# Performance work log

Hardware: AMD Instinct MI355X
Metric: run time of the kernel (lower is better)

The kernel has to match this reference:

```python
import jax, jax.numpy as jnp
import numpy as np

CLIP_DIM = 1024
X_DIM = 768
NUM_HEADS = 8
HEAD_DIM = X_DIM // NUM_HEADS
SCALE = HEAD_DIM ** -0.5
EPS1 = 1e-6  # custom channel-first LayerNorm
EPS2 = 1e-5  # nn.LayerNorm default


def setup_inputs() -> dict:
    key = jax.random.key(0)
    ks = jax.random.split(key, 12)
    B, H, W = 8, 32, 32
    d = X_DIM
    inp = {
        "x": jax.random.normal(ks[0], (B, H, W, d), jnp.float32),
        "clip_features": jax.random.normal(ks[1], (B, CLIP_DIM, 16, 16), jnp.float32),
        "conv_w": jax.random.normal(ks[2], (CLIP_DIM, d), jnp.float32) * (CLIP_DIM ** -0.5),
        "conv_b": jnp.zeros((d,), jnp.float32),
        "ln1_w": jnp.ones((d,), jnp.float32),
        "ln1_b": jnp.zeros((d,), jnp.float32),
        "wq": jax.random.normal(ks[3], (d, d), jnp.float32) * (d ** -0.5),
        "bq": jnp.zeros((d,), jnp.float32),
        "wk": jax.random.normal(ks[4], (d, d), jnp.float32) * (d ** -0.5),
        "bk": jnp.zeros((d,), jnp.float32),
        "wv": jax.random.normal(ks[5], (d, d), jnp.float32) * (d ** -0.5),
        "bv": jnp.zeros((d,), jnp.float32),
        "wo": jax.random.normal(ks[6], (d, d), jnp.float32) * (d ** -0.5),
        "bo": jnp.zeros((d,), jnp.float32),
        "ln2_w": jnp.ones((d,), jnp.float32),
        "ln2_b": jnp.zeros((d,), jnp.float32),
    }
    return inp


def _forward(x, clip_features, conv_w, conv_b, ln1_w, ln1_b,
             wq, bq, wk, bk, wv, bv, wo, bo, ln2_w, ln2_b):
    B, H, W, d = x.shape
    S = H * W
    # bilinear resize (align_corners=False == half-pixel, jax default)
    clip_r = jax.image.resize(clip_features, (B, CLIP_DIM, H, W), method="bilinear")
    # 1x1 conv: bchw,cd->bdhw
    c = jnp.einsum("bchw,cd->bdhw", clip_r, conv_w) + conv_b[None, :, None, None]
    # channel-first LayerNorm over dim 1
    u = c.mean(1, keepdims=True)
    s = ((c - u) ** 2).mean(1, keepdims=True)
    c = (c - u) * jax.lax.rsqrt(s + EPS1)
    c = ln1_w[None, :, None, None] * c + ln1_b[None, :, None, None]
    # to (B, S, d)
    q_in = jnp.transpose(c, (0, 2, 3, 1)).reshape(B, S, d)
    kv_in = x.reshape(B, S, d)
    # projections -> (B, h, S, hd)
    def heads(t):
        return jnp.transpose(t.reshape(B, S, NUM_HEADS, HEAD_DIM), (0, 2, 1, 3))
    q = heads(q_in @ wq + bq)
    k = heads(kv_in @ wk + bk)
    v = heads(kv_in @ wv + bv)
    scores = jnp.einsum("bhqd,bhkd->bhqk", q, k) * SCALE
    attn = jax.nn.softmax(scores, axis=-1)
    o = jnp.einsum("bhqk,bhkd->bhqd", attn, v)
    o = jnp.transpose(o, (0, 2, 1, 3)).reshape(B, S, d)
    o = o @ wo + bo
    # standard LayerNorm over last dim
    mu = o.mean(-1, keepdims=True)
    var = ((o - mu) ** 2).mean(-1, keepdims=True)
    o = (o - mu) * jax.lax.rsqrt(var + EPS2) * ln2_w + ln2_b
    return o.reshape(B, H, W, d)


def reference(x, clip_features, conv_w, conv_b, ln1_w, ln1_b,
              wq, bq, wk, bk, wv, bv, wo, bo, ln2_w, ln2_b):
    return _forward(x, clip_features, conv_w, conv_b, ln1_w, ln1_b,
                    wq, bq, wk, bk, wv, bv, wo, bo, ln2_w, ln2_b)
```

## Files before the change

kernel.cpp:

```cpp
#include <hip/hip_runtime.h>
#include <hip/hip_bf16.h>

typedef __attribute__((ext_vector_type(8))) short short8;
typedef __attribute__((ext_vector_type(4))) short short4v;
typedef __attribute__((ext_vector_type(4))) float floatx4;
typedef unsigned short u16;

__device__ __forceinline__ float b2f(u16 u) {
    unsigned int x = ((unsigned int)u) << 16;
    float f;
    __builtin_memcpy(&f, &x, 4);
    return f;
}
__device__ __forceinline__ u16 f2b(float f) {
    unsigned int x;
    __builtin_memcpy(&x, &f, 4);
    unsigned int lsb = (x >> 16) & 1u;
    x += 0x7fffu + lsb;
    return (u16)(x >> 16);
}

__device__ __forceinline__ void gload16(const u16* g, u16* l) {
    __builtin_amdgcn_global_load_lds(
        (const __attribute__((address_space(1))) void*)g,
        (__attribute__((address_space(3))) void*)l,
        16, 0, 0);
}

__global__ __launch_bounds__(256) void transpose_f2b(const float* __restrict__ in,
                                                     u16* __restrict__ out,
                                                     int R, int C, long ibs, long obs) {
    __shared__ float tile[32][33];
    int b = blockIdx.z;
    const float* ip = in + (long)b * ibs;
    u16* op = out + (long)b * obs;
    int c0 = blockIdx.x * 32, r0 = blockIdx.y * 32;
    int tx = threadIdx.x & 31, ty = threadIdx.x >> 5;
    for (int j = 0; j < 32; j += 8)
        tile[ty + j][tx] = ip[(long)(r0 + ty + j) * C + c0 + tx];
    __syncthreads();
    for (int j = 0; j < 32; j += 8)
        op[(long)(c0 + ty + j) * R + r0 + tx] = f2b(tile[tx][ty + j]);
}

__global__ __launch_bounds__(256) void transpose_w4(const float* __restrict__ w0,
                                                    const float* __restrict__ w1,
                                                    const float* __restrict__ w2,
                                                    const float* __restrict__ w3,
                                                    u16* __restrict__ outbase) {
    __shared__ float tile[32][33];
    int z = blockIdx.z;
    const float* ip = (z == 0) ? w0 : (z == 1) ? w1 : (z == 2) ? w2 : w3;
    u16* op = outbase + (long)z * 589824;
    int c0 = blockIdx.x * 32, r0 = blockIdx.y * 32;
    int tx = threadIdx.x & 31, ty = threadIdx.x >> 5;
    for (int j = 0; j < 32; j += 8)
        tile[ty + j][tx] = ip[(long)(r0 + ty + j) * 768 + c0 + tx];
    __syncthreads();
    for (int j = 0; j < 32; j += 8)
        op[(long)(c0 + ty + j) * 768 + r0 + tx] = f2b(tile[tx][ty + j]);
}

__global__ __launch_bounds__(256) void cast_f2b(const float* __restrict__ in,
                                                u16* __restrict__ out, int n8) {
    int i = blockIdx.x * 256 + threadIdx.x;
    if (i < n8) {
        float4 f0 = ((const float4*)in)[i * 2];
        float4 f1 = ((const float4*)in)[i * 2 + 1];
        short8 s;
        s[0] = (short)f2b(f0.x); s[1] = (short)f2b(f0.y);
        s[2] = (short)f2b(f0.z); s[3] = (short)f2b(f0.w);
        s[4] = (short)f2b(f1.x); s[5] = (short)f2b(f1.y);
        s[6] = (short)f2b(f1.z); s[7] = (short)f2b(f1.w);
        ((short8*)out)[i] = s;
    }
}

__global__ __launch_bounds__(256) void gemm_ld64(const u16* __restrict__ A,
                                                 const u16* __restrict__ Bt,
                                                 const float* __restrict__ bias,
                                                 u16* __restrict__ Cv,
                                                 int M, int N, int K, int ldc,
                                                 float oscale) {
    __shared__ __align__(16) u16 lA[128 * 64];
    __shared__ __align__(16) u16 lB[64 * 64];
    int tid = threadIdx.x, lane = tid & 63, w = tid >> 6;
    int m0 = blockIdx.x * 128, n0 = blockIdx.y * 64;
    floatx4 acc[2][4] = {};
    const int lr = lane & 15, kg = lane >> 4;
    int rt = tid >> 3, sl = ((tid & 7) ^ (rt & 7)) * 8;
    const u16* gA0 = &A[(long)(m0 + rt) * K + sl];
    const u16* gA1 = &A[(long)(m0 + 32 + rt) * K + sl];
    const u16* gA2 = &A[(long)(m0 + 64 + rt) * K + sl];
    const u16* gA3 = &A[(long)(m0 + 96 + rt) * K + sl];
    const u16* gB0 = &Bt[(long)(n0 + rt) * K + sl];
    const u16* gB1 = &Bt[(long)(n0 + 32 + rt) * K + sl];
    const int s0 = (kg ^ (lr & 7)) * 8;
    for (int k0 = 0; k0 < K; k0 += 64) {
        gload16(gA0 + k0, &lA[w * 512]);
        gload16(gA1 + k0, &lA[2048 + w * 512]);
        gload16(gA2 + k0, &lA[4096 + w * 512]);
        gload16(gA3 + k0, &lA[6144 + w * 512]);
        gload16(gB0 + k0, &lB[w * 512]);
        gload16(gB1 + k0, &lB[2048 + w * 512]);
        __syncthreads();
        #pragma unroll
        for (int ks = 0; ks < 2; ks++) {
            int sseg = s0 ^ (ks << 5);
            short8 a0 = *(const short8*)&lA[(w * 32 + lr) * 64 + sseg];
            short8 a1 = *(const short8*)&lA[(w * 32 + 16 + lr) * 64 + sseg];
            #pragma unroll
            for (int ni = 0; ni < 4; ni++) {
                short8 bf = *(const short8*)&lB[(ni * 16 + lr) * 64 + sseg];
                acc[0][ni] = __builtin_amdgcn_mfma_f32_16x16x32_bf16(a0, bf, acc[0][ni], 0, 0, 0);
                acc[1][ni] = __builtin_amdgcn_mfma_f32_16x16x32_bf16(a1, bf, acc[1][ni], 0, 0, 0);
            }
        }
        __syncthreads();
    }
    #pragma unroll
    for (int mi = 0; mi < 2; mi++)
        #pragma unroll
        for (int ni = 0; ni < 4; ni++) {
            int n = n0 + ni * 16 + lr;
            float bv = bias[n];
            #pragma unroll
            for (int r = 0; r < 4; r++) {
                int m = m0 + w * 32 + mi * 16 + kg * 4 + r;
                Cv[(long)m * ldc + n] = f2b((acc[mi][ni][r] + bv) * oscale);
            }
        }
}

__global__ __launch_bounds__(256) void gemm128kv(const u16* __restrict__ A,
                                                 const u16* __restrict__ Bt,
                                                 const float* __restrict__ biasA,
                                                 const float* __restrict__ biasB,
                                                 u16* __restrict__ Cv,
                                                 u16* __restrict__ vTout,
                                                 int M, int N, int K, int ldc) {
    __shared__ __align__(16) u16 lA[128 * 64];
    __shared__ __align__(16) u16 lB[128 * 64];
    int tid = threadIdx.x, lane = tid & 63, w = tid >> 6;
    int wr = w >> 1, wc = w & 1;
    int m0 = blockIdx.x * 128, n0 = blockIdx.y * 128;
    floatx4 acc[4][4] = {};
    const int lr = lane & 15, kg = lane >> 4;
    int rt = tid >> 3, sl = ((tid & 7) ^ (rt & 7)) * 8;
    const u16* gA0 = &A[(long)(m0 + rt) * K + sl];
    const u16* gA1 = &A[(long)(m0 + 32 + rt) * K + sl];
    const u16* gA2 = &A[(long)(m0 + 64 + rt) * K + sl];
    const u16* gA3 = &A[(long)(m0 + 96 + rt) * K + sl];
    const u16* gB0 = &Bt[(long)(n0 + rt) * K + sl];
    const u16* gB1 = &Bt[(long)(n0 + 32 + rt) * K + sl];
    const u16* gB2 = &Bt[(long)(n0 + 64 + rt) * K + sl];
    const u16* gB3 = &Bt[(long)(n0 + 96 + rt) * K + sl];
    const int s0 = (kg ^ (lr & 7)) * 8;
    for (int k0 = 0; k0 < K; k0 += 64) {
        gload16(gA0 + k0, &lA[w * 512]);
        gload16(gA1 + k0, &lA[2048 + w * 512]);
        gload16(gA2 + k0, &lA[4096 + w * 512]);
        gload16(gA3 + k0, &lA[6144 + w * 512]);
        gload16(gB0 + k0, &lB[w * 512]);
        gload16(gB1 + k0, &lB[2048 + w * 512]);
        gload16(gB2 + k0, &lB[4096 + w * 512]);
        gload16(gB3 + k0, &lB[6144 + w * 512]);
        __syncthreads();
        #pragma unroll
        for (int ks = 0; ks < 2; ks++) {
            int sseg = s0 ^ (ks << 5);
            short8 af[4], bf[4];
            #pragma unroll
            for (int mi = 0; mi < 4; mi++)
                af[mi] = *(const short8*)&lA[(wr * 64 + mi * 16 + lr) * 64 + sseg];
            #pragma unroll
            for (int ni = 0; ni < 4; ni++)
                bf[ni] = *(const short8*)&lB[(wc * 64 + ni * 16 + lr) * 64 + sseg];
            #pragma unroll
            for (int mi = 0; mi < 4; mi++)
                #pragma unroll
                for (int ni = 0; ni < 4; ni++)
                    acc[mi][ni] = __builtin_amdgcn_mfma_f32_16x16x32_bf16(af[mi], bf[ni], acc[mi][ni], 0, 0, 0);
        }
        __syncthreads();
    }
    #pragma unroll
    for (int mi = 0; mi < 4; mi++)
        #pragma unroll
        for (int ni = 0; ni < 4; ni++) {
            int n = n0 + wc * 64 + ni * 16 + lr;
            float bv = (n < 768) ? biasA[n] : biasB[n - 768];
            if (n >= 768) {
                int fg = n - 768;
                int h = fg / 96, f = fg - h * 96;
                int mb = m0 + wr * 64 + mi * 16 + kg * 4;
                long vrow = ((long)((m0 >> 10) * 8 + h) * 96 + f) * 1024 + (mb & 1023);
                short4v pk;
                #pragma unroll
                for (int r = 0; r < 4; r++) pk[r] = (short)f2b(acc[mi][ni][r] + bv);
                *(short4v*)&vTout[vrow] = pk;
            } else {
                #pragma unroll
                for (int r = 0; r < 4; r++) {
                    int m = m0 + wr * 64 + mi * 16 + kg * 4 + r;
                    Cv[(long)m * ldc + n] = f2b(acc[mi][ni][r] + bv);
                }
            }
        }
}

__global__ __launch_bounds__(256) void ln1_resize_w(const u16* __restrict__ t_lo,
                                                    const float* __restrict__ lnw,
                                                    const float* __restrict__ lnb,
                                                    u16* __restrict__ q_in) {
    int wv = threadIdx.x >> 6, lane = threadIdx.x & 63;
    int b = blockIdx.z, oh = blockIdx.y, ow = blockIdx.x * 4 + wv;
    float sy = oh * 0.5f - 0.25f;
    int iy = (int)floorf(sy);
    float fy = sy - (float)iy;
    int y0 = min(max(iy, 0), 15), y1 = min(max(iy + 1, 0), 15);
    float sx = ow * 0.5f - 0.25f;
    int ix = (int)floorf(sx);
    float fx = sx - (float)ix;
    int x0 = min(max(ix, 0), 15), x1 = min(max(ix + 1, 0), 15);
    float w00 = (1.f - fy) * (1.f - fx), w01 = (1.f - fy) * fx;
    float w10 = fy * (1.f - fx), w11 = fy * fx;
    long base = (long)b * 256 * 768;
    long i00 = base + (long)(y0 * 16 + x0) * 768;
    long i01 = base + (long)(y0 * 16 + x1) * 768;
    long i10 = base + (long)(y1 * 16 + x0) * 768;
    long i11 = base + (long)(y1 * 16 + x1) * 768;
    float v[12];
    float s = 0.f, sq = 0.f;
    #pragma unroll
    for (int j = 0; j < 3; j++) {
        int c0 = (j * 64 + lane) * 4;
        short4v a = *(const short4v*)&t_lo[i00 + c0];
        short4v c = *(const short4v*)&t_lo[i01 + c0];
        short4v d = *(const short4v*)&t_lo[i10 + c0];
        short4v e = *(const short4v*)&t_lo[i11 + c0];
        #pragma unroll
        for (int k = 0; k < 4; k++) {
            float val = w00 * b2f((u16)a[k]) + w01 * b2f((u16)c[k]) +
                        w10 * b2f((u16)d[k]) + w11 * b2f((u16)e[k]);
            v[j * 4 + k] = val;
            s += val;
            sq += val * val;
        }
    }
    #pragma unroll
    for (int off = 32; off >= 1; off >>= 1) {
        s += __shfl_xor(s, off);
        sq += __shfl_xor(sq, off);
    }
    float mean = s * (1.f / 768.f);
    float var = sq * (1.f / 768.f) - mean * mean;
    float rstd = rsqrtf(var + 1e-6f);
    long orow = ((long)b * 1024 + oh * 32 + ow) * 768;
    #pragma unroll
    for (int j = 0; j < 3; j++) {
        int c0 = (j * 64 + lane) * 4;
        float4 w4 = *(const float4*)&lnw[c0];
        float4 b4 = *(const float4*)&lnb[c0];
        short4v o;
        o[0] = (short)f2b((v[j * 4 + 0] - mean) * rstd * w4.x + b4.x);
        o[1] = (short)f2b((v[j * 4 + 1] - mean) * rstd * w4.y + b4.y);
        o[2] = (short)f2b((v[j * 4 + 2] - mean) * rstd * w4.z + b4.z);
        o[3] = (short)f2b((v[j * 4 + 3] - mean) * rstd * w4.w + b4.w);
        *(short4v*)&q_in[orow + c0] = o;
    }
}

#define PP 76
__global__ __launch_bounds__(512) void attn_kernel(const u16* __restrict__ Q,
                                                   const u16* __restrict__ Km,
                                                   const u16* __restrict__ Vt,
                                                   u16* __restrict__ O) {
    __shared__ __align__(16) u16 lK[2 * 4096];
    __shared__ __align__(16) u16 lKb[2 * 2048];
    __shared__ __align__(16) u16 lV[2 * 6144];
    __shared__ __align__(16) u16 lP[128 * PP];
    int tid = threadIdx.x, lane = tid & 63, w = tid >> 6;
    int L = blockIdx.x + (blockIdx.y << 3) + (blockIdx.z << 6);
    int b = L & 7, h = (L >> 3) & 7, qt = L >> 6;
    const int lr = lane & 15, kg = lane >> 4;

    long qrow = ((long)b * 1024 + qt * 128 + w * 16 + lr) * 768 + h * 96;
    short8 aq[3];
    for (int ks = 0; ks < 3; ks++) aq[ks] = *(const short8*)&Q[qrow + ks * 32 + kg * 8];

    floatx4 acco[6] = {};
    float lrun[4] = {0.f, 0.f, 0.f, 0.f};

    long kvbase = ((long)b * 1024) * 768 + h * 96;
    long vtbase = ((long)(b * 8 + h)) * 96 * 1024;

    const u16* gp[3];
    u16* lp[3];
    int gs[3], bs[3];
    #pragma unroll
    for (int i = 0; i < 3; i++) {
        int id = tid + i * 512;
        if (id < 512) {
            int row = id >> 3, lg = (id & 7) ^ (row & 7);
            lp[i] = &lK[id * 8];
            gp[i] = &Km[kvbase + (long)row * 768 + lg * 8];
            gs[i] = 64 * 768;
            bs[i] = 4096;
        } else if (id < 768) {
            int j = id - 512;
            int row = j >> 2, lg = (j & 3) ^ (row & 3);
            lp[i] = &lKb[j * 8];
            gp[i] = &Km[kvbase + (long)row * 768 + 64 + lg * 8];
            gs[i] = 64 * 768;
            bs[i] = 2048;
        } else {
            int j = id - 768;
            int f = j >> 3, lg = (j & 7) ^ (f & 7);
            lp[i] = &lV[j * 8];
            gp[i] = &Vt[vtbase + (long)f * 1024 + lg * 8];
            gs[i] = 64;
            bs[i] = 6144;
        }
    }

    const int sA = (kg ^ (lr & 7)) * 8;
    const int sB = (kg ^ (lr & 3)) * 8;

    #pragma unroll
    for (int i = 0; i < 3; i++) {
        gload16(gp[i], lp[i]);
        gp[i] += gs[i];
    }

    for (int kt = 0; kt < 16; kt++) {
        int cur = kt & 1, nxt = cur ^ 1;
        if (kt < 15) {
            #pragma unroll
            for (int i = 0; i < 3; i++) {
                gload16(gp[i], lp[i] + nxt * bs[i]);
                gp[i] += gs[i];
            }
            asm volatile("s_waitcnt vmcnt(3)" ::: "memory");
        } else {
            asm volatile("s_waitcnt vmcnt(0)" ::: "memory");
        }
        __builtin_amdgcn_sched_barrier(0);
        __builtin_amdgcn_s_barrier();

        const u16* K0 = &lK[cur * 4096];
        const u16* Kb0 = &lKb[cur * 2048];
        const u16* V0 = &lV[cur * 6144];

        floatx4 accs[4] = {};
        for (int ni = 0; ni < 4; ni++) {
            int rb = (ni * 16 + lr);
            short8 bk0 = *(const short8*)&K0[rb * 64 + sA];
            short8 bk1 = *(const short8*)&K0[rb * 64 + (sA ^ 32)];
            short8 bk2 = *(const short8*)&Kb0[rb * 32 + sB];
            accs[ni] = __builtin_amdgcn_mfma_f32_16x16x32_bf16(aq[0], bk0, accs[ni], 0, 0, 0);
            accs[ni] = __builtin_amdgcn_mfma_f32_16x16x32_bf16(aq[1], bk1, accs[ni], 0, 0, 0);
            accs[ni] = __builtin_amdgcn_mfma_f32_16x16x32_bf16(aq[2], bk2, accs[ni], 0, 0, 0);
        }

        for (int r = 0; r < 4; r++) {
            float p0 = __builtin_amdgcn_exp2f(accs[0][r]);
            float p1 = __builtin_amdgcn_exp2f(accs[1][r]);
            float p2 = __builtin_amdgcn_exp2f(accs[2][r]);
            float p3 = __builtin_amdgcn_exp2f(accs[3][r]);
            lrun[r] += (p0 + p1) + (p2 + p3);
            int prow = w * 16 + kg * 4 + r;
            lP[prow * PP + 0 + lr] = f2b(p0);
            lP[prow * PP + 16 + lr] = f2b(p1);
            lP[prow * PP + 32 + lr] = f2b(p2);
            lP[prow * PP + 48 + lr] = f2b(p3);
        }

        short8 ap0 = *(const short8*)&lP[(w * 16 + lr) * PP + kg * 8];
        short8 ap1 = *(const short8*)&lP[(w * 16 + lr) * PP + 32 + kg * 8];
        for (int nb = 0; nb < 6; nb++) {
            int fb = (nb * 16 + lr);
            short8 bv0 = *(const short8*)&V0[fb * 64 + sA];
            short8 bv1 = *(const short8*)&V0[fb * 64 + (sA ^ 32)];
            acco[nb] = __builtin_amdgcn_mfma_f32_16x16x32_bf16(ap0, bv0, acco[nb], 0, 0, 0);
            acco[nb] = __builtin_amdgcn_mfma_f32_16x16x32_bf16(ap1, bv1, acco[nb], 0, 0, 0);
        }
        __builtin_amdgcn_s_barrier();
    }

    #pragma unroll
    for (int r = 0; r < 4; r++)
        for (int off = 1; off < 16; off <<= 1) lrun[r] += __shfl_xor(lrun[r], off);
    float invl[4];
    #pragma unroll
    for (int r = 0; r < 4; r++) invl[r] = 1.0f / lrun[r];

    long obase = ((long)b * 1024 + qt * 128 + w * 16) * 768 + h * 96;
    for (int nb = 0; nb < 6; nb++)
        for (int r = 0; r < 4; r++) {
            float val = acco[nb][r] * invl[r];
            O[obase + (long)(kg * 4 + r) * 768 + nb * 16 + lr] = f2b(val);
        }
}

__global__ __launch_bounds__(256) void ln2_w(const u16* __restrict__ o,
                                             const float* __restrict__ lnw,
                                             const float* __restrict__ lnb,
                                             float* __restrict__ out) {
    int wv = threadIdx.x >> 6, lane = threadIdx.x & 63;
    long row = (long)blockIdx.x * 4 + wv;
    long base = row * 768;
    float v[12];
    float s = 0.f, sq = 0.f;
    #pragma unroll
    for (int j = 0; j < 3; j++) {
        int c0 = (j * 64 + lane) * 4;
        short4v a = *(const short4v*)&o[base + c0];
        #pragma unroll
        for (int k = 0; k < 4; k++) {
            float val = b2f((u16)a[k]);
            v[j * 4 + k] = val;
            s += val;
            sq += val * val;
        }
    }
    #pragma unroll
    for (int off = 32; off >= 1; off >>= 1) {
        s += __shfl_xor(s, off);
        sq += __shfl_xor(sq, off);
    }
    float mean = s * (1.f / 768.f);
    float var = sq * (1.f / 768.f) - mean * mean;
    float rstd = rsqrtf(var + 1e-5f);
    #pragma unroll
    for (int j = 0; j < 3; j++) {
        int c0 = (j * 64 + lane) * 4;
        float4 w4 = *(const float4*)&lnw[c0];
        float4 b4 = *(const float4*)&lnb[c0];
        float4 r4;
        r4.x = (v[j * 4 + 0] - mean) * rstd * w4.x + b4.x;
        r4.y = (v[j * 4 + 1] - mean) * rstd * w4.y + b4.y;
        r4.z = (v[j * 4 + 2] - mean) * rstd * w4.z + b4.z;
        r4.w = (v[j * 4 + 3] - mean) * rstd * w4.w + b4.w;
        *(float4*)&out[base + c0] = r4;
    }
}

extern "C" void kernel_launch(void* const* d_in, const int* in_sizes, int n_in,
                              void* d_out, int out_size, void* d_ws, size_t ws_size,
                              hipStream_t stream) {
    const float* x       = (const float*)d_in[0];
    const float* clip    = (const float*)d_in[1];
    const float* conv_w  = (const float*)d_in[2];
    const float* conv_b  = (const float*)d_in[3];
    const float* ln1_w   = (const float*)d_in[4];
    const float* ln1_b   = (const float*)d_in[5];
    const float* wq      = (const float*)d_in[6];
    const float* bq      = (const float*)d_in[7];
    const float* wk      = (const float*)d_in[8];
    const float* bk      = (const float*)d_in[9];
    const float* wv      = (const float*)d_in[10];
    const float* bv      = (const float*)d_in[11];
    const float* wo      = (const float*)d_in[12];
    const float* bo      = (const float*)d_in[13];
    const float* ln2_w_  = (const float*)d_in[14];
    const float* ln2_b_  = (const float*)d_in[15];
    float* out = (float*)d_out;

    u16* ws = (u16*)d_ws;
    u16* clipT   = ws;
    u16* convwT  = clipT + 2097152;
    u16* wqT     = convwT + 786432;
    u16* wkT     = wqT + 589824;
    u16* wvT     = wkT + 589824;
    u16* woT     = wvT + 589824;
    u16* t_lo    = woT + 589824;
    u16* q_in    = t_lo + 1572864;
    u16* qb      = q_in + 6291456;
    u16* kb      = qb + 6291456;
    u16* vT      = kb + 6291456;
    u16* xb      = q_in;
    u16* attno   = q_in;
    u16* obuf    = qb;

    const float QSCALE = 0.10206207261596575f * 1.4426950408889634f;

    transpose_f2b<<<dim3(8, 32, 8), 256, 0, stream>>>(clip, clipT, 1024, 256, 262144, 262144);
    transpose_f2b<<<dim3(24, 32, 1), 256, 0, stream>>>(conv_w, convwT, 1024, 768, 0, 0);
    transpose_w4<<<dim3(24, 24, 4), 256, 0, stream>>>(wq, wk, wv, wo, wqT);

    gemm_ld64<<<dim3(16, 12), 256, 0, stream>>>(clipT, convwT, conv_b, t_lo,
                                                2048, 768, 1024, 768, 1.0f);

    ln1_resize_w<<<dim3(8, 32, 8), 256, 0, stream>>>(t_lo, ln1_w, ln1_b, q_in);

    gemm_ld64<<<dim3(64, 12), 256, 0, stream>>>(q_in, wqT, bq, qb, 8192, 768, 768, 768, QSCALE);
    cast_f2b<<<3072, 256, 0, stream>>>(x, xb, 786432);

    gemm128kv<<<dim3(64, 12), 256, 0, stream>>>(xb, wkT, bk, bv, kb, vT, 8192, 1536, 768, 768);

    attn_kernel<<<dim3(8, 8, 8), 512, 0, stream>>>(qb, kb, vT, attno);

    gemm_ld64<<<dim3(64, 12), 256, 0, stream>>>(attno, woT, bo, obuf, 8192, 768, 768, 768, 1.0f);

    ln2_w<<<2048, 256, 0, stream>>>(obuf, ln2_w_, ln2_b_, out);
}
```

Measured before the change: 143.8 us.

## Merge transpose launches into one kernel and raise wave priority around attention MFMAs

```diff
diff --git a/kernel.cpp b/kernel.cpp
--- a/kernel.cpp
+++ b/kernel.cpp
@@ -27,38 +27,46 @@
         16, 0, 0);
 }
 
-__global__ __launch_bounds__(256) void transpose_f2b(const float* __restrict__ in,
-                                                     u16* __restrict__ out,
-                                                     int R, int C, long ibs, long obs) {
+__global__ __launch_bounds__(256) void transpose_all(const float* __restrict__ clip,
+                                                     const float* __restrict__ conv_w,
+                                                     const float* __restrict__ w0,
+                                                     const float* __restrict__ w1,
+                                                     const float* __restrict__ w2,
+                                                     const float* __restrict__ w3,
+                                                     u16* __restrict__ clipT,
+                                                     u16* __restrict__ convwT,
+                                                     u16* __restrict__ wT) {
     __shared__ float tile[32][33];
-    int b = blockIdx.z;
-    const float* ip = in + (long)b * ibs;
-    u16* op = out + (long)b * obs;
-    int c0 = blockIdx.x * 32, r0 = blockIdx.y * 32;
+    int id = blockIdx.x;
+    const float* ip;
+    u16* op;
+    int R, C, c0, r0;
+    if (id < 2048) {
+        int b = id >> 8, rem = id & 255;
+        R = 1024; C = 256;
+        c0 = (rem & 7) * 32; r0 = (rem >> 3) * 32;
+        ip = clip + (long)b * 262144;
+        op = clipT + (long)b * 262144;
+    } else if (id < 2816) {
+        int i2 = id - 2048;
+        R = 1024; C = 768;
+        c0 = (i2 % 24) * 32; r0 = (i2 / 24) * 32;
+        ip = conv_w;
+        op = convwT;
+    } else {
+        int i3 = id - 2816;
+        int z = i3 / 576, rem = i3 % 576;
+        R = 768; C = 768;
+        c0 = (rem % 24) * 32; r0 = (rem / 24) * 32;
+        ip = (z == 0) ? w0 : (z == 1) ? w1 : (z == 2) ? w2 : w3;
+        op = wT + (long)z * 589824;
+    }
     int tx = threadIdx.x & 31, ty = threadIdx.x >> 5;
     for (int j = 0; j < 32; j += 8)
         tile[ty + j][tx] = ip[(long)(r0 + ty + j) * C + c0 + tx];
     __syncthreads();
     for (int j = 0; j < 32; j += 8)
         op[(long)(c0 + ty + j) * R + r0 + tx] = f2b(tile[tx][ty + j]);
-}
-
-__global__ __launch_bounds__(256) void transpose_w4(const float* __restrict__ w0,
-                                                    const float* __restrict__ w1,
-                                                    const float* __restrict__ w2,
-                                                    const float* __restrict__ w3,
-                                                    u16* __restrict__ outbase) {
-    __shared__ float tile[32][33];
-    int z = blockIdx.z;
-    const float* ip = (z == 0) ? w0 : (z == 1) ? w1 : (z == 2) ? w2 : w3;
-    u16* op = outbase + (long)z * 589824;
-    int c0 = blockIdx.x * 32, r0 = blockIdx.y * 32;
-    int tx = threadIdx.x & 31, ty = threadIdx.x >> 5;
-    for (int j = 0; j < 32; j += 8)
-        tile[ty + j][tx] = ip[(long)(r0 + ty + j) * 768 + c0 + tx];
-    __syncthreads();
-    for (int j = 0; j < 32; j += 8)
-        op[(long)(c0 + ty + j) * 768 + r0 + tx] = f2b(tile[tx][ty + j]);
 }
 
 __global__ __launch_bounds__(256) void cast_f2b(const float* __restrict__ in,
@@ -353,6 +361,7 @@
         const u16* V0 = &lV[cur * 6144];
 
         floatx4 accs[4] = {};
+        __builtin_amdgcn_s_setprio(1);
         for (int ni = 0; ni < 4; ni++) {
             int rb = (ni * 16 + lr);
             short8 bk0 = *(const short8*)&K0[rb * 64 + sA];
@@ -362,6 +371,7 @@
             accs[ni] = __builtin_amdgcn_mfma_f32_16x16x32_bf16(aq[1], bk1, accs[ni], 0, 0, 0);
             accs[ni] = __builtin_amdgcn_mfma_f32_16x16x32_bf16(aq[2], bk2, accs[ni], 0, 0, 0);
         }
+        __builtin_amdgcn_s_setprio(0);
 
         for (int r = 0; r < 4; r++) {
             float p0 = __builtin_amdgcn_exp2f(accs[0][r]);
@@ -378,6 +388,7 @@
 
         short8 ap0 = *(const short8*)&lP[(w * 16 + lr) * PP + kg * 8];
         short8 ap1 = *(const short8*)&lP[(w * 16 + lr) * PP + 32 + kg * 8];
+        __builtin_amdgcn_s_setprio(1);
         for (int nb = 0; nb < 6; nb++) {
             int fb = (nb * 16 + lr);
             short8 bv0 = *(const short8*)&V0[fb * 64 + sA];
@@ -385,6 +396,7 @@
             acco[nb] = __builtin_amdgcn_mfma_f32_16x16x32_bf16(ap0, bv0, acco[nb], 0, 0, 0);
             acco[nb] = __builtin_amdgcn_mfma_f32_16x16x32_bf16(ap1, bv1, acco[nb], 0, 0, 0);
         }
+        __builtin_amdgcn_s_setprio(0);
         __builtin_amdgcn_s_barrier();
     }
 
@@ -485,9 +497,8 @@
 
     const float QSCALE = 0.10206207261596575f * 1.4426950408889634f;
 
-    transpose_f2b<<<dim3(8, 32, 8), 256, 0, stream>>>(clip, clipT, 1024, 256, 262144, 262144);
-    transpose_f2b<<<dim3(24, 32, 1), 256, 0, stream>>>(conv_w, convwT, 1024, 768, 0, 0);
-    transpose_w4<<<dim3(24, 24, 4), 256, 0, stream>>>(wq, wk, wv, wo, wqT);
+    transpose_all<<<5120, 256, 0, stream>>>(clip, conv_w, wq, wk, wv, wo,
+                                            clipT, convwT, wqT);
 
     gemm_ld64<<<dim3(16, 12), 256, 0, stream>>>(clipT, convwT, conv_b, t_lo,
                                                 2048, 768, 1024, 768, 1.0f);
```

After: 138.0 us. -4.0%, faster.
